# Optimization experiments

Measured on AMD Instinct MI355X. Metric: run time of the kernel, lower is better.

The kernel has to match this reference:

```python
import jax, jax.numpy as jnp
import numpy as np

B, N, D, H = 2, 2048, 1024, 16
DH = D // H  # 64


def setup_inputs() -> dict:
    key = jax.random.key(0)
    k1, k2, k3, k4, k5 = jax.random.split(key, 5)
    x = jax.random.normal(k1, (B, N, D), dtype=jnp.float32)
    # per-head kqv Linear weights, stacked: [H, D, 3*DH] (acts as x @ W)
    W_kqv = jax.random.normal(k2, (H, D, 3 * DH), dtype=jnp.float32) * 0.02
    b_kqv = jax.random.normal(k3, (H, 3 * DH), dtype=jnp.float32) * 0.02
    W_proj = jax.random.normal(k4, (D, D), dtype=jnp.float32) * 0.02
    b_proj = jax.random.normal(k5, (D,), dtype=jnp.float32) * 0.02
    return {"x": x, "W_kqv": W_kqv, "b_kqv": b_kqv, "W_proj": W_proj, "b_proj": b_proj}


def reference(x, W_kqv, b_kqv, W_proj, b_proj):
    # per-head projections, all heads batched: [B, H, N, 3*DH]
    kqv = jnp.einsum('bnd,hde->bhne', x, W_kqv) + b_kqv[None, :, None, :]
    # original chunk order is k, q, v
    k, q, v = jnp.split(kqv, 3, axis=-1)  # each [B, H, N, DH]
    # scores: A = q @ k^T / sqrt(DH)  -> [B, H, N, N]
    A = jnp.einsum('bhnd,bhmd->bhnm', q, k) / jnp.sqrt(jnp.asarray(DH, x.dtype))
    causal = jnp.tril(jnp.ones((N, N), dtype=bool))
    A = jnp.where(causal[None, None, :, :], A, -jnp.inf)
    attn = jax.nn.softmax(A, axis=-1)
    sa = jnp.einsum('bhnm,bhmd->bhnd', attn, v)          # [B, H, N, DH]
    sa = sa.transpose(0, 2, 1, 3).reshape(B, N, D)        # concat heads
    out = sa @ W_proj.T + b_proj                          # output projection
    return out
```

## Files before the change

### kernel.cpp

```cpp
#include <hip/hip_runtime.h>
#include <hip/hip_bf16.h>
#include <cstdint>
#include <cstddef>

#define B_  2
#define N_  2048
#define D_  1024
#define H_  16
#define DH_ 64
#define E3_ 192

typedef __attribute__((ext_vector_type(8))) short short8;
typedef __attribute__((ext_vector_type(8))) unsigned short ushort8v;
typedef __attribute__((ext_vector_type(4))) float floatx4;

static __device__ __forceinline__ unsigned short f2bf(float f) {
  union { float f; unsigned u; } c; c.f = f;
  unsigned r = c.u + 0x7fffu + ((c.u >> 16) & 1u);
  return (unsigned short)(r >> 16);
}

#define MFMA(a,b,c) __builtin_amdgcn_mfma_f32_16x16x32_bf16((a),(b),(c),0,0,0)

#define GL_LDS16(g, l) __builtin_amdgcn_global_load_lds( \
    (const __attribute__((address_space(1))) void*)(g),  \
    (__attribute__((address_space(3))) void*)(l), 16, 0, 0)

__global__ __launch_bounds__(256) void k_f2bf(const float* __restrict__ in,
                                              unsigned short* __restrict__ out, int n8) {
  int i = blockIdx.x * blockDim.x + threadIdx.x;
  if (i >= n8) return;
  const float4* p = (const float4*)in + (size_t)i * 2;
  float4 a = p[0], b = p[1];
  ushort8v o;
  o[0]=f2bf(a.x); o[1]=f2bf(a.y); o[2]=f2bf(a.z); o[3]=f2bf(a.w);
  o[4]=f2bf(b.x); o[5]=f2bf(b.y); o[6]=f2bf(b.z); o[7]=f2bf(b.w);
  *((ushort8v*)out + i) = o;
}

__global__ __launch_bounds__(256) void k_twkqv(const float* __restrict__ W,
                                               unsigned short* __restrict__ Wt) {
  __shared__ float tile[64][65];
  int h = blockIdx.z, cat = blockIdx.y, e0 = cat * 64, d0 = blockIdx.x * 64;
  int t = threadIdx.x;
  const float* Wp = W + (size_t)h * D_ * E3_;
  int dr = t >> 2, ec = (t & 3) * 16;
#pragma unroll
  for (int j = 0; j < 16; j += 4) {
    float4 wv = *(const float4*)&Wp[(size_t)(d0 + dr) * E3_ + e0 + ec + j];
    tile[dr][ec + j + 0] = wv.x; tile[dr][ec + j + 1] = wv.y;
    tile[dr][ec + j + 2] = wv.z; tile[dr][ec + j + 3] = wv.w;
  }
  __syncthreads();
  int er = t >> 2, dc = (t & 3) * 16;
  ushort8v o0, o1;
#pragma unroll
  for (int j = 0; j < 8; j++) o0[j] = f2bf(tile[dc + j][er]);
#pragma unroll
  for (int j = 0; j < 8; j++) o1[j] = f2bf(tile[dc + 8 + j][er]);
  size_t o = ((size_t)(cat * 1024 + h * 64 + er)) * D_ + d0 + dc;
  *(ushort8v*)&Wt[o]     = o0;
  *(ushort8v*)&Wt[o + 8] = o1;
}

__global__ __launch_bounds__(256) void k_qkv(const unsigned short* __restrict__ Xb,
                                             const unsigned short* __restrict__ Wt,
                                             const float* __restrict__ bkqv,
                                             unsigned short* __restrict__ Qb,
                                             unsigned short* __restrict__ Kb,
                                             unsigned short* __restrict__ Vt) {
  __shared__ unsigned short Alds[2][128 * 32];
  __shared__ unsigned short Blds[2][128 * 32];
  int t = threadIdx.x;
  int m0 = blockIdx.x * 128, c0 = blockIdx.y * 128;
  int wave = t >> 6, lane = t & 63, quad = lane >> 4, l16 = lane & 15;
  int wm = (wave >> 1) * 64, wn = (wave & 1) * 64;
  floatx4 acc[4][4];
#pragma unroll
  for (int i = 0; i < 4; i++)
#pragma unroll
    for (int j = 0; j < 4; j++) acc[i][j] = (floatx4){0.f, 0.f, 0.f, 0.f};

  const unsigned short* gA = Xb + (size_t)(m0 + wave * 32 + (lane >> 2)) * D_ + (lane & 3) * 8;
  const unsigned short* gB = Wt + (size_t)(c0 + wave * 32 + (lane >> 2)) * D_ + (lane & 3) * 8;
  unsigned short* lA0 = &Alds[0][(wave * 32) * 32];
  unsigned short* lA1 = &Alds[1][(wave * 32) * 32];
  unsigned short* lB0 = &Blds[0][(wave * 32) * 32];
  unsigned short* lB1 = &Blds[1][(wave * 32) * 32];

  for (int k0 = 0; k0 < D_; k0 += 64) {
    GL_LDS16(gA + k0,                 lA0);
    GL_LDS16(gA + k0 + 16 * D_,       lA0 + 16 * 32);
    GL_LDS16(gA + k0 + 32,            lA1);
    GL_LDS16(gA + k0 + 32 + 16 * D_,  lA1 + 16 * 32);
    GL_LDS16(gB + k0,                 lB0);
    GL_LDS16(gB + k0 + 16 * D_,       lB0 + 16 * 32);
    GL_LDS16(gB + k0 + 32,            lB1);
    GL_LDS16(gB + k0 + 32 + 16 * D_,  lB1 + 16 * 32);
    __syncthreads();
#pragma unroll
    for (int kk = 0; kk < 2; kk++) {
      short8 a[4], b[4];
#pragma unroll
      for (int mi = 0; mi < 4; mi++) a[mi] = *(const short8*)&Alds[kk][(wm + mi * 16 + l16) * 32 + quad * 8];
#pragma unroll
      for (int ni = 0; ni < 4; ni++) b[ni] = *(const short8*)&Blds[kk][(wn + ni * 16 + l16) * 32 + quad * 8];
#pragma unroll
      for (int mi = 0; mi < 4; mi++)
#pragma unroll
        for (int ni = 0; ni < 4; ni++) acc[mi][ni] = MFMA(a[mi], b[ni], acc[mi][ni]);
    }
    __syncthreads();
  }

  int cat = c0 >> 10;
#pragma unroll
  for (int mi = 0; mi < 4; mi++)
#pragma unroll
    for (int ni = 0; ni < 4; ni++) {
      int colp = c0 + wn + ni * 16 + l16;
      int h = (colp >> 6) & 15;
      int e = colp & 63;
      int grow = m0 + wm + mi * 16 + quad * 4;
      int b = grow >> 11, n0 = grow & (N_ - 1);
      int bh = b * H_ + h;
      float bias = bkqv[h * E3_ + cat * 64 + e];
      floatx4 v = acc[mi][ni];
      if (cat == 0) {
        size_t base = ((size_t)bh * N_ + n0) * DH_ + e;
#pragma unroll
        for (int r = 0; r < 4; r++) Kb[base + (size_t)r * DH_] = f2bf(v[r] + bias);
      } else if (cat == 1) {
        size_t base = ((size_t)bh * N_ + n0) * DH_ + e;
#pragma unroll
        for (int r = 0; r < 4; r++) Qb[base + (size_t)r * DH_] = f2bf((v[r] + bias) * 0.125f);
      } else {
        ushort4 pk;
        pk.x = f2bf(v[0] + bias); pk.y = f2bf(v[1] + bias);
        pk.z = f2bf(v[2] + bias); pk.w = f2bf(v[3] + bias);
        *(ushort4*)&Vt[((size_t)bh * DH_ + e) * N_ + n0] = pk;
      }
    }
}

#define PSTR 72
__global__ __launch_bounds__(256) void k_flash(const unsigned short* __restrict__ Qb,
                                               const unsigned short* __restrict__ Kb,
                                               const unsigned short* __restrict__ Vt,
                                               unsigned short* __restrict__ sab) {
  int bh = blockIdx.x;
  int y = blockIdx.y;
  int qb = (y < 8) ? y : 23 - y;
  int q0b = qb * 128;
  int wave = threadIdx.x >> 6;
  int lane = threadIdx.x & 63, quad = lane >> 4, l16 = lane & 15;
  const unsigned short* Qp = Qb + (size_t)bh * N_ * DH_;
  const unsigned short* Kp = Kb + (size_t)bh * N_ * DH_;
  const unsigned short* Vp = Vt + (size_t)bh * DH_ * N_;
  __shared__ unsigned short Klds[2 * 64 * 32];
  __shared__ unsigned short Vlds[2 * 64 * 32];
  __shared__ unsigned short Plds[4][16 * PSTR];
  unsigned short* P = Plds[wave];

  short8 qf[2][2];
#pragma unroll
  for (int st = 0; st < 2; st++) {
    int q0 = q0b + st * 64 + wave * 16;
    qf[st][0] = *(const short8*)&Qp[(q0 + l16) * DH_ + quad * 8];
    qf[st][1] = *(const short8*)&Qp[(q0 + l16) * DH_ + 32 + quad * 8];
  }
  const unsigned short* gK = Kp + (size_t)(wave * 16 + (lane >> 2)) * DH_ + (lane & 3) * 8;
  const unsigned short* gV = Vp + (size_t)(wave * 16 + (lane >> 2)) * N_ + (lane & 3) * 8;
  unsigned short* lK = &Klds[(wave * 16) * 32];
  unsigned short* lV = &Vlds[(wave * 16) * 32];

  floatx4 O[2][4];
  float lr[2][4];
#pragma unroll
  for (int st = 0; st < 2; st++)
#pragma unroll
    for (int r = 0; r < 4; r++) { O[st][r] = (floatx4){0.f, 0.f, 0.f, 0.f}; lr[st][r] = 0.f; }

  for (int kv0 = 0; kv0 <= q0b + 64; kv0 += 64) {
    GL_LDS16(gK + (size_t)kv0 * DH_,      lK);
    GL_LDS16(gK + (size_t)kv0 * DH_ + 32, lK + 64 * 32);
    GL_LDS16(gV + kv0,                    lV);
    GL_LDS16(gV + kv0 + 32,               lV + 64 * 32);
    __syncthreads();

    short8 kf0[4], kf1[4], vf0[4], vf1[4];
#pragma unroll
    for (int c = 0; c < 4; c++) {
      kf0[c] = *(const short8*)&Klds[(c * 16 + l16) * 32 + quad * 8];
      kf1[c] = *(const short8*)&Klds[(64 + c * 16 + l16) * 32 + quad * 8];
      vf0[c] = *(const short8*)&Vlds[(c * 16 + l16) * 32 + quad * 8];
      vf1[c] = *(const short8*)&Vlds[(64 + c * 16 + l16) * 32 + quad * 8];
    }
#pragma unroll
    for (int st = 0; st < 2; st++) {
      if (st == 0 && kv0 > q0b) continue;
      floatx4 s[4];
#pragma unroll
      for (int c = 0; c < 4; c++) {
        s[c] = (floatx4){0.f, 0.f, 0.f, 0.f};
        s[c] = MFMA(qf[st][0], kf0[c], s[c]);
        s[c] = MFMA(qf[st][1], kf1[c], s[c]);
      }
      if (kv0 == q0b + st * 64) {
#pragma unroll
        for (int c = 0; c < 4; c++)
#pragma unroll
          for (int r = 0; r < 4; r++) {
            int row = wave * 16 + quad * 4 + r;
            if (c * 16 + l16 > row) s[c][r] = -1e30f;
          }
      }
#pragma unroll
      for (int c = 0; c < 4; c++)
#pragma unroll
        for (int r = 0; r < 4; r++)
          s[c][r] = __builtin_amdgcn_exp2f(s[c][r] * 1.44269504f);
#pragma unroll
      for (int r = 0; r < 4; r++)
        lr[st][r] += (s[0][r] + s[1][r]) + (s[2][r] + s[3][r]);
#pragma unroll
      for (int c = 0; c < 4; c++)
#pragma unroll
        for (int r = 0; r < 4; r++)
          P[(quad * 4 + r) * PSTR + c * 16 + l16] = f2bf(s[c][r]);
      __asm__ volatile("s_waitcnt lgkmcnt(0)" ::: "memory");
      short8 pa0 = *(const short8*)&P[l16 * PSTR + quad * 8];
      short8 pa1 = *(const short8*)&P[l16 * PSTR + 32 + quad * 8];
      __asm__ volatile("" ::: "memory");
#pragma unroll
      for (int dt = 0; dt < 4; dt++) {
        O[st][dt] = MFMA(pa0, vf0[dt], O[st][dt]);
        O[st][dt] = MFMA(pa1, vf1[dt], O[st][dt]);
      }
    }
    __syncthreads();
  }
#pragma unroll
  for (int m = 1; m < 16; m <<= 1)
#pragma unroll
    for (int st = 0; st < 2; st++)
#pragma unroll
      for (int r = 0; r < 4; r++) lr[st][r] += __shfl_xor(lr[st][r], m);

  int b = bh >> 4, h = bh & 15;
#pragma unroll
  for (int st = 0; st < 2; st++) {
    int q0 = q0b + st * 64 + wave * 16;
#pragma unroll
    for (int r = 0; r < 4; r++) {
      float inv = 1.0f / lr[st][r];
      size_t base = ((size_t)b * N_ + q0 + quad * 4 + r) * D_ + h * DH_;
#pragma unroll
      for (int dt = 0; dt < 4; dt++) sab[base + dt * 16 + l16] = f2bf(O[st][dt][r] * inv);
    }
  }
}

__global__ __launch_bounds__(256) void k_proj(const unsigned short* __restrict__ sab,
                                              const unsigned short* __restrict__ Wpb,
                                              const float* __restrict__ bproj,
                                              float* __restrict__ out) {
  __shared__ unsigned short Alds[2][128 * 32];
  __shared__ unsigned short Blds[2][64 * 32];
  int t = threadIdx.x;
  int m0 = blockIdx.x * 128, c0 = blockIdx.y * 64;
  int wave = t >> 6, lane = t & 63, quad = lane >> 4, l16 = lane & 15;
  int wm = (wave >> 1) * 64, wn = (wave & 1) * 32;
  floatx4 acc[4][2];
#pragma unroll
  for (int i = 0; i < 4; i++) { acc[i][0] = (floatx4){0,0,0,0}; acc[i][1] = (floatx4){0,0,0,0}; }

  const unsigned short* gA = sab + (size_t)(m0 + wave * 32 + (lane >> 2)) * D_ + (lane & 3) * 8;
  const unsigned short* gB = Wpb + (size_t)(c0 + wave * 16 + (lane >> 2)) * D_ + (lane & 3) * 8;
  unsigned short* lA0 = &Alds[0][(wave * 32) * 32];
  unsigned short* lA1 = &Alds[1][(wave * 32) * 32];
  unsigned short* lB0 = &Blds[0][(wave * 16) * 32];
  unsigned short* lB1 = &Blds[1][(wave * 16) * 32];

  for (int k0 = 0; k0 < D_; k0 += 64) {
    GL_LDS16(gA + k0,                lA0);
    GL_LDS16(gA + k0 + 16 * D_,      lA0 + 16 * 32);
    GL_LDS16(gA + k0 + 32,           lA1);
    GL_LDS16(gA + k0 + 32 + 16 * D_, lA1 + 16 * 32);
    GL_LDS16(gB + k0,                lB0);
    GL_LDS16(gB + k0 + 32,           lB1);
    __syncthreads();
#pragma unroll
    for (int kk = 0; kk < 2; kk++) {
      short8 a[4], b[2];
#pragma unroll
      for (int mi = 0; mi < 4; mi++) a[mi] = *(const short8*)&Alds[kk][(wm + mi * 16 + l16) * 32 + quad * 8];
#pragma unroll
      for (int ni = 0; ni < 2; ni++) b[ni] = *(const short8*)&Blds[kk][(wn + ni * 16 + l16) * 32 + quad * 8];
#pragma unroll
      for (int mi = 0; mi < 4; mi++)
#pragma unroll
        for (int ni = 0; ni < 2; ni++) acc[mi][ni] = MFMA(a[mi], b[ni], acc[mi][ni]);
    }
    __syncthreads();
  }
#pragma unroll
  for (int mi = 0; mi < 4; mi++)
#pragma unroll
    for (int ni = 0; ni < 2; ni++) {
      int col = c0 + wn + ni * 16 + l16;
      int grow = m0 + wm + mi * 16 + quad * 4;
      float bias = bproj[col];
#pragma unroll
      for (int r = 0; r < 4; r++)
        out[(size_t)(grow + r) * D_ + col] = acc[mi][ni][r] + bias;
    }
}

extern "C" void kernel_launch(void* const* d_in, const int* in_sizes, int n_in,
                              void* d_out, int out_size, void* d_ws, size_t ws_size,
                              hipStream_t stream) {
  const float* x     = (const float*)d_in[0];
  const float* Wkqv  = (const float*)d_in[1];
  const float* bkqv  = (const float*)d_in[2];
  const float* Wproj = (const float*)d_in[3];
  const float* bproj = (const float*)d_in[4];
  float* out = (float*)d_out;

  char* w = (char*)d_ws;
  unsigned short* Xb  = (unsigned short*)(w);
  unsigned short* Wt  = (unsigned short*)(w + (8u  << 20));
  unsigned short* Wpb = (unsigned short*)(w + (14u << 20));
  unsigned short* Qb  = (unsigned short*)(w + (16u << 20));
  unsigned short* Kb  = (unsigned short*)(w + (24u << 20));
  unsigned short* Vt  = (unsigned short*)(w + (32u << 20));
  unsigned short* sa  = (unsigned short*)(w + (40u << 20));

  k_f2bf<<<(B_ * N_ * D_ / 8 + 255) / 256, 256, 0, stream>>>(x, Xb, B_ * N_ * D_ / 8);
  k_twkqv<<<dim3(D_ / 64, 3, H_), 256, 0, stream>>>(Wkqv, Wt);
  k_f2bf<<<(D_ * D_ / 8 + 255) / 256, 256, 0, stream>>>(Wproj, Wpb, D_ * D_ / 8);
  k_qkv<<<dim3(B_ * N_ / 128, 3072 / 128), 256, 0, stream>>>(Xb, Wt, bkqv, Qb, Kb, Vt);
  k_flash<<<dim3(B_ * H_, N_ / 128), 256, 0, stream>>>(Qb, Kb, Vt, sa);
  k_proj<<<dim3(B_ * N_ / 128, D_ / 64), 256, 0, stream>>>(sa, Wpb, bproj, out);
}
```

Before: 207.5 us.

## Shrink flash query tile to 64 rows and double-buffer K/V loads

The flash attention kernel now gives each block 64 query rows instead of 128, doubling the grid, and uses a four-group interleaved mapping to balance causal work across blocks. K/V tiles are double-buffered in LDS so the next tile's global-to-LDS load is issued while the current tile is being computed, which removes one barrier per iteration. The aim is better occupancy and load balance plus hidden load latency. In exchange, each K/V tile is now fetched by twice as many blocks and LDS use grows.

Measured after the change: 188.6 us. 1.1x faster.

```diff
diff --git a/kernel.cpp b/kernel.cpp
--- a/kernel.cpp
+++ b/kernel.cpp
@@ -149,115 +149,107 @@
                                                const unsigned short* __restrict__ Vt,
                                                unsigned short* __restrict__ sab) {
   int bh = blockIdx.x;
-  int y = blockIdx.y;
-  int qb = (y < 8) ? y : 23 - y;
-  int q0b = qb * 128;
+  int yr = blockIdx.y, g = yr >> 3, o = yr & 7;
+  int qb = (g == 0) ? o : (g == 1) ? 31 - o : (g == 2) ? 8 + o : 23 - o;
+  int q0b = qb * 64;
   int wave = threadIdx.x >> 6;
   int lane = threadIdx.x & 63, quad = lane >> 4, l16 = lane & 15;
   const unsigned short* Qp = Qb + (size_t)bh * N_ * DH_;
   const unsigned short* Kp = Kb + (size_t)bh * N_ * DH_;
   const unsigned short* Vp = Vt + (size_t)bh * DH_ * N_;
-  __shared__ unsigned short Klds[2 * 64 * 32];
-  __shared__ unsigned short Vlds[2 * 64 * 32];
+  __shared__ unsigned short Klds[2][2 * 64 * 32];
+  __shared__ unsigned short Vlds[2][2 * 64 * 32];
   __shared__ unsigned short Plds[4][16 * PSTR];
   unsigned short* P = Plds[wave];
 
-  short8 qf[2][2];
-#pragma unroll
-  for (int st = 0; st < 2; st++) {
-    int q0 = q0b + st * 64 + wave * 16;
-    qf[st][0] = *(const short8*)&Qp[(q0 + l16) * DH_ + quad * 8];
-    qf[st][1] = *(const short8*)&Qp[(q0 + l16) * DH_ + 32 + quad * 8];
-  }
+  int q0w = q0b + wave * 16;
+  short8 qf0 = *(const short8*)&Qp[(q0w + l16) * DH_ + quad * 8];
+  short8 qf1 = *(const short8*)&Qp[(q0w + l16) * DH_ + 32 + quad * 8];
+
   const unsigned short* gK = Kp + (size_t)(wave * 16 + (lane >> 2)) * DH_ + (lane & 3) * 8;
   const unsigned short* gV = Vp + (size_t)(wave * 16 + (lane >> 2)) * N_ + (lane & 3) * 8;
-  unsigned short* lK = &Klds[(wave * 16) * 32];
-  unsigned short* lV = &Vlds[(wave * 16) * 32];
-
-  floatx4 O[2][4];
-  float lr[2][4];
-#pragma unroll
-  for (int st = 0; st < 2; st++)
-#pragma unroll
-    for (int r = 0; r < 4; r++) { O[st][r] = (floatx4){0.f, 0.f, 0.f, 0.f}; lr[st][r] = 0.f; }
-
-  for (int kv0 = 0; kv0 <= q0b + 64; kv0 += 64) {
-    GL_LDS16(gK + (size_t)kv0 * DH_,      lK);
-    GL_LDS16(gK + (size_t)kv0 * DH_ + 32, lK + 64 * 32);
-    GL_LDS16(gV + kv0,                    lV);
-    GL_LDS16(gV + kv0 + 32,               lV + 64 * 32);
-    __syncthreads();
-
-    short8 kf0[4], kf1[4], vf0[4], vf1[4];
+  int lofs = (wave * 16) * 32;
+
+  floatx4 O[4];
+  float lr[4];
+#pragma unroll
+  for (int r = 0; r < 4; r++) { O[r] = (floatx4){0.f, 0.f, 0.f, 0.f}; lr[r] = 0.f; }
+
+  int nt = (q0b >> 6) + 1;
+  GL_LDS16(gK,      &Klds[0][lofs]);
+  GL_LDS16(gK + 32, &Klds[0][lofs + 64 * 32]);
+  GL_LDS16(gV,      &Vlds[0][lofs]);
+  GL_LDS16(gV + 32, &Vlds[0][lofs + 64 * 32]);
+
+  for (int i = 0; i < nt; i++) {
+    int buf = i & 1;
+    __syncthreads();
+    if (i + 1 < nt) {
+      int kvn = (i + 1) << 6;
+      GL_LDS16(gK + (size_t)kvn * DH_,      &Klds[buf ^ 1][lofs]);
+      GL_LDS16(gK + (size_t)kvn * DH_ + 32, &Klds[buf ^ 1][lofs + 64 * 32]);
+      GL_LDS16(gV + kvn,                    &Vlds[buf ^ 1][lofs]);
+      GL_LDS16(gV + kvn + 32,               &Vlds[buf ^ 1][lofs + 64 * 32]);
+    }
+    short8 kf[4][2], vf[4][2];
 #pragma unroll
     for (int c = 0; c < 4; c++) {
-      kf0[c] = *(const short8*)&Klds[(c * 16 + l16) * 32 + quad * 8];
-      kf1[c] = *(const short8*)&Klds[(64 + c * 16 + l16) * 32 + quad * 8];
-      vf0[c] = *(const short8*)&Vlds[(c * 16 + l16) * 32 + quad * 8];
-      vf1[c] = *(const short8*)&Vlds[(64 + c * 16 + l16) * 32 + quad * 8];
-    }
-#pragma unroll
-    for (int st = 0; st < 2; st++) {
-      if (st == 0 && kv0 > q0b) continue;
-      floatx4 s[4];
-#pragma unroll
-      for (int c = 0; c < 4; c++) {
-        s[c] = (floatx4){0.f, 0.f, 0.f, 0.f};
-        s[c] = MFMA(qf[st][0], kf0[c], s[c]);
-        s[c] = MFMA(qf[st][1], kf1[c], s[c]);
-      }
-      if (kv0 == q0b + st * 64) {
-#pragma unroll
-        for (int c = 0; c < 4; c++)
-#pragma unroll
-          for (int r = 0; r < 4; r++) {
-            int row = wave * 16 + quad * 4 + r;
-            if (c * 16 + l16 > row) s[c][r] = -1e30f;
-          }
-      }
+      kf[c][0] = *(const short8*)&Klds[buf][(c * 16 + l16) * 32 + quad * 8];
+      kf[c][1] = *(const short8*)&Klds[buf][(64 + c * 16 + l16) * 32 + quad * 8];
+      vf[c][0] = *(const short8*)&Vlds[buf][(c * 16 + l16) * 32 + quad * 8];
+      vf[c][1] = *(const short8*)&Vlds[buf][(64 + c * 16 + l16) * 32 + quad * 8];
+    }
+    floatx4 s[4];
+#pragma unroll
+    for (int c = 0; c < 4; c++) {
+      s[c] = (floatx4){0.f, 0.f, 0.f, 0.f};
+      s[c] = MFMA(qf0, kf[c][0], s[c]);
+      s[c] = MFMA(qf1, kf[c][1], s[c]);
+    }
+    if (i == nt - 1) {
 #pragma unroll
       for (int c = 0; c < 4; c++)
 #pragma unroll
-        for (int r = 0; r < 4; r++)
-          s[c][r] = __builtin_amdgcn_exp2f(s[c][r] * 1.44269504f);
+        for (int r = 0; r < 4; r++) {
+          int row = wave * 16 + quad * 4 + r;
+          if (c * 16 + l16 > row) s[c][r] = -1e30f;
+        }
+    }
+#pragma unroll
+    for (int c = 0; c < 4; c++)
 #pragma unroll
       for (int r = 0; r < 4; r++)
-        lr[st][r] += (s[0][r] + s[1][r]) + (s[2][r] + s[3][r]);
-#pragma unroll
-      for (int c = 0; c < 4; c++)
-#pragma unroll
-        for (int r = 0; r < 4; r++)
-          P[(quad * 4 + r) * PSTR + c * 16 + l16] = f2bf(s[c][r]);
-      __asm__ volatile("s_waitcnt lgkmcnt(0)" ::: "memory");
-      short8 pa0 = *(const short8*)&P[l16 * PSTR + quad * 8];
-      short8 pa1 = *(const short8*)&P[l16 * PSTR + 32 + quad * 8];
-      __asm__ volatile("" ::: "memory");
-#pragma unroll
-      for (int dt = 0; dt < 4; dt++) {
-        O[st][dt] = MFMA(pa0, vf0[dt], O[st][dt]);
-        O[st][dt] = MFMA(pa1, vf1[dt], O[st][dt]);
-      }
-    }
-    __syncthreads();
+        s[c][r] = __builtin_amdgcn_exp2f(s[c][r] * 1.44269504f);
+#pragma unroll
+    for (int r = 0; r < 4; r++)
+      lr[r] += (s[0][r] + s[1][r]) + (s[2][r] + s[3][r]);
+#pragma unroll
+    for (int c = 0; c < 4; c++)
+#pragma unroll
+      for (int r = 0; r < 4; r++)
+        P[(quad * 4 + r) * PSTR + c * 16 + l16] = f2bf(s[c][r]);
+    __asm__ volatile("s_waitcnt lgkmcnt(0)" ::: "memory");
+    short8 pa0 = *(const short8*)&P[l16 * PSTR + quad * 8];
+    short8 pa1 = *(const short8*)&P[l16 * PSTR + 32 + quad * 8];
+    __asm__ volatile("" ::: "memory");
+#pragma unroll
+    for (int dt = 0; dt < 4; dt++) {
+      O[dt] = MFMA(pa0, vf[dt][0], O[dt]);
+      O[dt] = MFMA(pa1, vf[dt][1], O[dt]);
+    }
   }
 #pragma unroll
   for (int m = 1; m < 16; m <<= 1)
 #pragma unroll
-    for (int st = 0; st < 2; st++)
-#pragma unroll
-      for (int r = 0; r < 4; r++) lr[st][r] += __shfl_xor(lr[st][r], m);
+    for (int r = 0; r < 4; r++) lr[r] += __shfl_xor(lr[r], m);
 
   int b = bh >> 4, h = bh & 15;
 #pragma unroll
-  for (int st = 0; st < 2; st++) {
-    int q0 = q0b + st * 64 + wave * 16;
-#pragma unroll
-    for (int r = 0; r < 4; r++) {
-      float inv = 1.0f / lr[st][r];
-      size_t base = ((size_t)b * N_ + q0 + quad * 4 + r) * D_ + h * DH_;
-#pragma unroll
-      for (int dt = 0; dt < 4; dt++) sab[base + dt * 16 + l16] = f2bf(O[st][dt][r] * inv);
-    }
+  for (int r = 0; r < 4; r++) {
+    float inv = 1.0f / lr[r];
+    size_t base = ((size_t)b * N_ + q0w + quad * 4 + r) * D_ + h * DH_;
+#pragma unroll
+    for (int dt = 0; dt < 4; dt++) sab[base + dt * 16 + l16] = f2bf(O[dt][r] * inv);
   }
 }
 
@@ -340,6 +332,6 @@
   k_twkqv<<<dim3(D_ / 64, 3, H_), 256, 0, stream>>>(Wkqv, Wt);
   k_f2bf<<<(D_ * D_ / 8 + 255) / 256, 256, 0, stream>>>(Wproj, Wpb, D_ * D_ / 8);
   k_qkv<<<dim3(B_ * N_ / 128, 3072 / 128), 256, 0, stream>>>(Xb, Wt, bkqv, Qb, Kb, Vt);
-  k_flash<<<dim3(B_ * H_, N_ / 128), 256, 0, stream>>>(Qb, Kb, Vt, sa);
+  k_flash<<<dim3(B_ * H_, N_ / 64), 256, 0, stream>>>(Qb, Kb, Vt, sa);
   k_proj<<<dim3(B_ * N_ / 128, D_ / 64), 256, 0, stream>>>(sa, Wpb, bproj, out);
 }
```

## Split KV tiles across wave pairs in flash kernel and shrink proj tiles

Applied to the files above, without the earlier changes.

The flash kernel now handles 64 query rows per block instead of 128. The two wave pairs each process alternating KV tiles, and their partial outputs and row sums are combined through LDS at the end. The q-block ordering is reworked to balance causal work across a grid twice as large, and the projection GEMM uses 64x64 tiles for more blocks. This raises parallelism and occupancy across CUs, at the cost of an extra LDS reduction, an extra barrier, and less K/V reuse per block.

New measurement: 189.9 us. 1.09x faster.

```diff
diff --git a/kernel.cpp b/kernel.cpp
--- a/kernel.cpp
+++ b/kernel.cpp
@@ -149,30 +149,30 @@
                                                const unsigned short* __restrict__ Vt,
                                                unsigned short* __restrict__ sab) {
   int bh = blockIdx.x;
-  int y = blockIdx.y;
-  int qb = (y < 8) ? y : 23 - y;
-  int q0b = qb * 128;
+  int yr = blockIdx.y, g4 = yr >> 3, o = yr & 7;
+  int qb = (g4 == 0) ? o : (g4 == 1) ? 31 - o : (g4 == 2) ? 8 + o : 23 - o;
+  int q0b = qb * 64;
   int wave = threadIdx.x >> 6;
+  int grp = wave >> 1, sub = wave & 1;
   int lane = threadIdx.x & 63, quad = lane >> 4, l16 = lane & 15;
   const unsigned short* Qp = Qb + (size_t)bh * N_ * DH_;
   const unsigned short* Kp = Kb + (size_t)bh * N_ * DH_;
   const unsigned short* Vp = Vt + (size_t)bh * DH_ * N_;
-  __shared__ unsigned short Klds[2 * 64 * 32];
-  __shared__ unsigned short Vlds[2 * 64 * 32];
+  __shared__ unsigned short Klds[2][2 * 64 * 32];
+  __shared__ unsigned short Vlds[2][2 * 64 * 32];
   __shared__ unsigned short Plds[4][16 * PSTR];
   unsigned short* P = Plds[wave];
 
   short8 qf[2][2];
 #pragma unroll
   for (int st = 0; st < 2; st++) {
-    int q0 = q0b + st * 64 + wave * 16;
-    qf[st][0] = *(const short8*)&Qp[(q0 + l16) * DH_ + quad * 8];
-    qf[st][1] = *(const short8*)&Qp[(q0 + l16) * DH_ + 32 + quad * 8];
+    int qw = q0b + sub * 32 + st * 16;
+    qf[st][0] = *(const short8*)&Qp[(qw + l16) * DH_ + quad * 8];
+    qf[st][1] = *(const short8*)&Qp[(qw + l16) * DH_ + 32 + quad * 8];
   }
   const unsigned short* gK = Kp + (size_t)(wave * 16 + (lane >> 2)) * DH_ + (lane & 3) * 8;
   const unsigned short* gV = Vp + (size_t)(wave * 16 + (lane >> 2)) * N_ + (lane & 3) * 8;
-  unsigned short* lK = &Klds[(wave * 16) * 32];
-  unsigned short* lV = &Vlds[(wave * 16) * 32];
+  int lofs = (wave * 16) * 32;
 
   floatx4 O[2][4];
   float lr[2][4];
@@ -181,82 +181,116 @@
 #pragma unroll
     for (int r = 0; r < 4; r++) { O[st][r] = (floatx4){0.f, 0.f, 0.f, 0.f}; lr[st][r] = 0.f; }
 
-  for (int kv0 = 0; kv0 <= q0b + 64; kv0 += 64) {
-    GL_LDS16(gK + (size_t)kv0 * DH_,      lK);
-    GL_LDS16(gK + (size_t)kv0 * DH_ + 32, lK + 64 * 32);
-    GL_LDS16(gV + kv0,                    lV);
-    GL_LDS16(gV + kv0 + 32,               lV + 64 * 32);
-    __syncthreads();
-
-    short8 kf0[4], kf1[4], vf0[4], vf1[4];
-#pragma unroll
-    for (int c = 0; c < 4; c++) {
-      kf0[c] = *(const short8*)&Klds[(c * 16 + l16) * 32 + quad * 8];
-      kf1[c] = *(const short8*)&Klds[(64 + c * 16 + l16) * 32 + quad * 8];
-      vf0[c] = *(const short8*)&Vlds[(c * 16 + l16) * 32 + quad * 8];
-      vf1[c] = *(const short8*)&Vlds[(64 + c * 16 + l16) * 32 + quad * 8];
-    }
+  int nt = qb + 1, npairs = (nt + 1) >> 1;
+  for (int j = 0; j < npairs; j++) {
+    if (j) __syncthreads();
+    int t0 = 2 * j;
+    {
+      size_t ko = (size_t)(t0 * 64) * DH_;
+      GL_LDS16(gK + ko,          &Klds[0][lofs]);
+      GL_LDS16(gK + ko + 32,     &Klds[0][lofs + 64 * 32]);
+      GL_LDS16(gV + t0 * 64,      &Vlds[0][lofs]);
+      GL_LDS16(gV + t0 * 64 + 32, &Vlds[0][lofs + 64 * 32]);
+    }
+    if (t0 + 1 < nt) {
+      size_t ko = (size_t)((t0 + 1) * 64) * DH_;
+      GL_LDS16(gK + ko,          &Klds[1][lofs]);
+      GL_LDS16(gK + ko + 32,     &Klds[1][lofs + 64 * 32]);
+      GL_LDS16(gV + (t0+1) * 64,      &Vlds[1][lofs]);
+      GL_LDS16(gV + (t0+1) * 64 + 32, &Vlds[1][lofs + 64 * 32]);
+    }
+    __syncthreads();
+    int t = t0 + grp;
+    if (t < nt) {
+      short8 kf[4][2], vf[4][2];
+#pragma unroll
+      for (int c = 0; c < 4; c++) {
+        kf[c][0] = *(const short8*)&Klds[grp][(c * 16 + l16) * 32 + quad * 8];
+        kf[c][1] = *(const short8*)&Klds[grp][(64 + c * 16 + l16) * 32 + quad * 8];
+        vf[c][0] = *(const short8*)&Vlds[grp][(c * 16 + l16) * 32 + quad * 8];
+        vf[c][1] = *(const short8*)&Vlds[grp][(64 + c * 16 + l16) * 32 + quad * 8];
+      }
+#pragma unroll
+      for (int st = 0; st < 2; st++) {
+        floatx4 s[4];
+#pragma unroll
+        for (int c = 0; c < 4; c++) {
+          s[c] = (floatx4){0.f, 0.f, 0.f, 0.f};
+          s[c] = MFMA(qf[st][0], kf[c][0], s[c]);
+          s[c] = MFMA(qf[st][1], kf[c][1], s[c]);
+        }
+        if (t == nt - 1) {
+#pragma unroll
+          for (int c = 0; c < 4; c++)
+#pragma unroll
+            for (int r = 0; r < 4; r++) {
+              int row = sub * 32 + st * 16 + quad * 4 + r;
+              if (c * 16 + l16 > row) s[c][r] = -1e30f;
+            }
+        }
+#pragma unroll
+        for (int c = 0; c < 4; c++)
+#pragma unroll
+          for (int r = 0; r < 4; r++)
+            s[c][r] = __builtin_amdgcn_exp2f(s[c][r] * 1.44269504f);
+#pragma unroll
+        for (int r = 0; r < 4; r++)
+          lr[st][r] += (s[0][r] + s[1][r]) + (s[2][r] + s[3][r]);
+#pragma unroll
+        for (int c = 0; c < 4; c++)
+#pragma unroll
+          for (int r = 0; r < 4; r++)
+            P[(quad * 4 + r) * PSTR + c * 16 + l16] = f2bf(s[c][r]);
+        __asm__ volatile("s_waitcnt lgkmcnt(0)" ::: "memory");
+        short8 pa0 = *(const short8*)&P[l16 * PSTR + quad * 8];
+        short8 pa1 = *(const short8*)&P[l16 * PSTR + 32 + quad * 8];
+        __asm__ volatile("" ::: "memory");
+#pragma unroll
+        for (int dt = 0; dt < 4; dt++) {
+          O[st][dt] = MFMA(pa0, vf[dt][0], O[st][dt]);
+          O[st][dt] = MFMA(pa1, vf[dt][1], O[st][dt]);
+        }
+      }
+    }
+  }
+#pragma unroll
+  for (int m = 1; m < 16; m <<= 1)
+#pragma unroll
+    for (int st = 0; st < 2; st++)
+#pragma unroll
+      for (int r = 0; r < 4; r++) lr[st][r] += __shfl_xor(lr[st][r], m);
+
+  __syncthreads();
+  float* OF = (float*)&Klds[0][0];
+  float* LF = (float*)&Vlds[0][0];
+  if (wave >= 2) {
+#pragma unroll
+    for (int st = 0; st < 2; st++)
+#pragma unroll
+      for (int dt = 0; dt < 4; dt++)
+        *(floatx4*)&OF[(((sub * 2 + st) * 4 + dt) << 8) + lane * 4] = O[st][dt];
+    if (l16 == 0)
+#pragma unroll
+      for (int st = 0; st < 2; st++)
+#pragma unroll
+        for (int r = 0; r < 4; r++) LF[(sub * 2 + st) * 16 + quad * 4 + r] = lr[st][r];
+  }
+  __syncthreads();
+  if (wave < 2) {
+    int b = bh >> 4, h = bh & 15;
 #pragma unroll
     for (int st = 0; st < 2; st++) {
-      if (st == 0 && kv0 > q0b) continue;
-      floatx4 s[4];
-#pragma unroll
-      for (int c = 0; c < 4; c++) {
-        s[c] = (floatx4){0.f, 0.f, 0.f, 0.f};
-        s[c] = MFMA(qf[st][0], kf0[c], s[c]);
-        s[c] = MFMA(qf[st][1], kf1[c], s[c]);
+#pragma unroll
+      for (int dt = 0; dt < 4; dt++)
+        O[st][dt] += *(const floatx4*)&OF[(((wave * 2 + st) * 4 + dt) << 8) + lane * 4];
+#pragma unroll
+      for (int r = 0; r < 4; r++) {
+        float lt = lr[st][r] + LF[(wave * 2 + st) * 16 + quad * 4 + r];
+        float inv = 1.0f / lt;
+        size_t base = ((size_t)b * N_ + q0b + wave * 32 + st * 16 + quad * 4 + r) * D_ + h * DH_;
+#pragma unroll
+        for (int dt = 0; dt < 4; dt++) sab[base + dt * 16 + l16] = f2bf(O[st][dt][r] * inv);
       }
-      if (kv0 == q0b + st * 64) {
-#pragma unroll
-        for (int c = 0; c < 4; c++)
-#pragma unroll
-          for (int r = 0; r < 4; r++) {
-            int row = wave * 16 + quad * 4 + r;
-            if (c * 16 + l16 > row) s[c][r] = -1e30f;
-          }
-      }
-#pragma unroll
-      for (int c = 0; c < 4; c++)
-#pragma unroll
-        for (int r = 0; r < 4; r++)
-          s[c][r] = __builtin_amdgcn_exp2f(s[c][r] * 1.44269504f);
-#pragma unroll
-      for (int r = 0; r < 4; r++)
-        lr[st][r] += (s[0][r] + s[1][r]) + (s[2][r] + s[3][r]);
-#pragma unroll
-      for (int c = 0; c < 4; c++)
-#pragma unroll
-        for (int r = 0; r < 4; r++)
-          P[(quad * 4 + r) * PSTR + c * 16 + l16] = f2bf(s[c][r]);
-      __asm__ volatile("s_waitcnt lgkmcnt(0)" ::: "memory");
-      short8 pa0 = *(const short8*)&P[l16 * PSTR + quad * 8];
-      short8 pa1 = *(const short8*)&P[l16 * PSTR + 32 + quad * 8];
-      __asm__ volatile("" ::: "memory");
-#pragma unroll
-      for (int dt = 0; dt < 4; dt++) {
-        O[st][dt] = MFMA(pa0, vf0[dt], O[st][dt]);
-        O[st][dt] = MFMA(pa1, vf1[dt], O[st][dt]);
-      }
-    }
-    __syncthreads();
-  }
-#pragma unroll
-  for (int m = 1; m < 16; m <<= 1)
-#pragma unroll
-    for (int st = 0; st < 2; st++)
-#pragma unroll
-      for (int r = 0; r < 4; r++) lr[st][r] += __shfl_xor(lr[st][r], m);
-
-  int b = bh >> 4, h = bh & 15;
-#pragma unroll
-  for (int st = 0; st < 2; st++) {
-    int q0 = q0b + st * 64 + wave * 16;
-#pragma unroll
-    for (int r = 0; r < 4; r++) {
-      float inv = 1.0f / lr[st][r];
-      size_t base = ((size_t)b * N_ + q0 + quad * 4 + r) * D_ + h * DH_;
-#pragma unroll
-      for (int dt = 0; dt < 4; dt++) sab[base + dt * 16 + l16] = f2bf(O[st][dt][r] * inv);
     }
   }
 }
@@ -265,47 +299,45 @@
                                               const unsigned short* __restrict__ Wpb,
                                               const float* __restrict__ bproj,
                                               float* __restrict__ out) {
-  __shared__ unsigned short Alds[2][128 * 32];
+  __shared__ unsigned short Alds[2][64 * 32];
   __shared__ unsigned short Blds[2][64 * 32];
   int t = threadIdx.x;
-  int m0 = blockIdx.x * 128, c0 = blockIdx.y * 64;
+  int m0 = blockIdx.x * 64, c0 = blockIdx.y * 64;
   int wave = t >> 6, lane = t & 63, quad = lane >> 4, l16 = lane & 15;
-  int wm = (wave >> 1) * 64, wn = (wave & 1) * 32;
-  floatx4 acc[4][2];
-#pragma unroll
-  for (int i = 0; i < 4; i++) { acc[i][0] = (floatx4){0,0,0,0}; acc[i][1] = (floatx4){0,0,0,0}; }
-
-  const unsigned short* gA = sab + (size_t)(m0 + wave * 32 + (lane >> 2)) * D_ + (lane & 3) * 8;
+  int wm = (wave >> 1) * 32, wn = (wave & 1) * 32;
+  floatx4 acc[2][2];
+#pragma unroll
+  for (int i = 0; i < 2; i++) { acc[i][0] = (floatx4){0,0,0,0}; acc[i][1] = (floatx4){0,0,0,0}; }
+
+  const unsigned short* gA = sab + (size_t)(m0 + wave * 16 + (lane >> 2)) * D_ + (lane & 3) * 8;
   const unsigned short* gB = Wpb + (size_t)(c0 + wave * 16 + (lane >> 2)) * D_ + (lane & 3) * 8;
-  unsigned short* lA0 = &Alds[0][(wave * 32) * 32];
-  unsigned short* lA1 = &Alds[1][(wave * 32) * 32];
+  unsigned short* lA0 = &Alds[0][(wave * 16) * 32];
+  unsigned short* lA1 = &Alds[1][(wave * 16) * 32];
   unsigned short* lB0 = &Blds[0][(wave * 16) * 32];
   unsigned short* lB1 = &Blds[1][(wave * 16) * 32];
 
   for (int k0 = 0; k0 < D_; k0 += 64) {
-    GL_LDS16(gA + k0,                lA0);
-    GL_LDS16(gA + k0 + 16 * D_,      lA0 + 16 * 32);
-    GL_LDS16(gA + k0 + 32,           lA1);
-    GL_LDS16(gA + k0 + 32 + 16 * D_, lA1 + 16 * 32);
-    GL_LDS16(gB + k0,                lB0);
-    GL_LDS16(gB + k0 + 32,           lB1);
+    GL_LDS16(gA + k0,      lA0);
+    GL_LDS16(gA + k0 + 32, lA1);
+    GL_LDS16(gB + k0,      lB0);
+    GL_LDS16(gB + k0 + 32, lB1);
     __syncthreads();
 #pragma unroll
     for (int kk = 0; kk < 2; kk++) {
-      short8 a[4], b[2];
-#pragma unroll
-      for (int mi = 0; mi < 4; mi++) a[mi] = *(const short8*)&Alds[kk][(wm + mi * 16 + l16) * 32 + quad * 8];
+      short8 a[2], b[2];
+#pragma unroll
+      for (int mi = 0; mi < 2; mi++) a[mi] = *(const short8*)&Alds[kk][(wm + mi * 16 + l16) * 32 + quad * 8];
 #pragma unroll
       for (int ni = 0; ni < 2; ni++) b[ni] = *(const short8*)&Blds[kk][(wn + ni * 16 + l16) * 32 + quad * 8];
 #pragma unroll
-      for (int mi = 0; mi < 4; mi++)
+      for (int mi = 0; mi < 2; mi++)
 #pragma unroll
         for (int ni = 0; ni < 2; ni++) acc[mi][ni] = MFMA(a[mi], b[ni], acc[mi][ni]);
     }
     __syncthreads();
   }
 #pragma unroll
-  for (int mi = 0; mi < 4; mi++)
+  for (int mi = 0; mi < 2; mi++)
 #pragma unroll
     for (int ni = 0; ni < 2; ni++) {
       int col = c0 + wn + ni * 16 + l16;
@@ -340,6 +372,6 @@
   k_twkqv<<<dim3(D_ / 64, 3, H_), 256, 0, stream>>>(Wkqv, Wt);
   k_f2bf<<<(D_ * D_ / 8 + 255) / 256, 256, 0, stream>>>(Wproj, Wpb, D_ * D_ / 8);
   k_qkv<<<dim3(B_ * N_ / 128, 3072 / 128), 256, 0, stream>>>(Xb, Wt, bkqv, Qb, Kb, Vt);
-  k_flash<<<dim3(B_ * H_, N_ / 128), 256, 0, stream>>>(Qb, Kb, Vt, sa);
-  k_proj<<<dim3(B_ * N_ / 128, D_ / 64), 256, 0, stream>>>(sa, Wpb, bproj, out);
-}
+  k_flash<<<dim3(B_ * H_, N_ / 64), 256, 0, stream>>>(Qb, Kb, Vt, sa);
+  k_proj<<<dim3(B_ * N_ / 64, D_ / 64), 256, 0, stream>>>(sa, Wpb, bproj, out);
+}
```
